# Kernel tuning notes

Measured on AMD Instinct MI355X. Metric: run time of the kernel, lower is better.

Reference implementation:

```python
import jax, jax.numpy as jnp
import numpy as np
import math

B, N, F, H = 16, 256, 1024, 16
HD = F // H  # head_dim = 64
NEG = -9e15


def setup_inputs() -> dict:
    key = jax.random.key(0)
    ks = jax.random.split(key, 12)
    s = 0.02
    return {
        "obj_feats": jax.random.normal(ks[0], (B, N, F), jnp.float32),
        "cross_feats": jax.random.normal(ks[1], (B, N, F), jnp.float32),
        "adj_matrix": jax.random.randint(ks[2], (B, N, N), 0, 2, jnp.int32),
        "label_biases_att": jax.random.normal(ks[3], (B, N, N), jnp.float32),
        "Wq": jax.random.normal(ks[4], (F, F), jnp.float32) * s,
        "bq": jnp.zeros((F,), jnp.float32),
        "Wk": jax.random.normal(ks[5], (F, F), jnp.float32) * s,
        "bk": jnp.zeros((F,), jnp.float32),
        "Wv": jax.random.normal(ks[6], (F, F), jnp.float32) * s,
        "bv": jnp.zeros((F,), jnp.float32),
        # grouped 1x1 conv: out=F, groups=H, in_per_group=F -> weight [F, F]
        "Wo": jax.random.normal(ks[7], (F, F), jnp.float32) * s,
        "bo": jnp.zeros((F,), jnp.float32),
    }


def reference(obj_feats, cross_feats, adj_matrix, label_biases_att,
              Wq, bq, Wk, bk, Wv, bv, Wo, bo):
    # projections (torch Linear: x @ W.T + b)
    q = (jnp.einsum('bnf,gf->bng', obj_feats, Wq) + bq).reshape(B, N, H, HD)
    k = (jnp.einsum('bnf,gf->bng', cross_feats, Wk) + bk).reshape(B, N, H, HD)
    v = jnp.einsum('bnf,gf->bng', cross_feats, Wv) + bv          # [B, N, F] (NOT split per head)

    scale = 1.0 / math.sqrt(float(HD))
    att = jnp.einsum('bqhd,bkhd->bqhk', q, k) * scale            # [B, Nq, H, Nk]

    # adjacency mask broadcast over heads + label bias (both indexed [b, q, k])
    mask = (adj_matrix > 0)[:, :, None, :]                       # [B, Nq, 1, Nk]
    att = jnp.where(mask, att, NEG) + label_biases_att[:, :, None, :]

    p = jax.nn.softmax(att, axis=-1)                             # softmax over keys

    # weighted sum against un-split values: [B, Nq, H, Nk] x [B, Nk, F]
    out = jnp.einsum('bqhk,bkf->bqhf', p, v)                     # [B, Nq, H, F]

    # grouped 1x1 conv: group h maps its F input channels -> HD output channels
    Wo_g = Wo.reshape(H, HD, F)
    out = jnp.einsum('bqhf,hdf->bqhd', out, Wo_g) + bo.reshape(H, HD)
    out = out.reshape(B, N, F)

    att_mean = p.sum(axis=2) / H                                 # [B, Nq, Nk]
    return out, att_mean
```

## Files before the change

### kernel.cpp

```cpp
#include <hip/hip_runtime.h>

#define NEGF -9e15f

typedef __attribute__((ext_vector_type(8))) unsigned short u16x8;
typedef __attribute__((ext_vector_type(8))) short          s16x8;
typedef __attribute__((ext_vector_type(4))) float          f32x4;

__device__ __forceinline__ unsigned short f2bf(float x) {
  union { float f; unsigned int u; } c; c.f = x;
  unsigned int r = c.u + 0x7fffu + ((c.u >> 16) & 1u);
  return (unsigned short)(r >> 16);
}
__device__ __forceinline__ float bf2f(unsigned short v) {
  union { float f; unsigned int u; } c; c.u = ((unsigned int)v) << 16;
  return c.f;
}

__device__ __forceinline__ void gload16(const void* g, void* l) {
  __builtin_amdgcn_global_load_lds(
      (const __attribute__((address_space(1))) unsigned int*)g,
      (__attribute__((address_space(3))) unsigned int*)l, 16, 0, 0);
}

__global__ __launch_bounds__(256) void cvt2_bf16(
    const float* __restrict__ a, const float* __restrict__ b,
    unsigned short* __restrict__ oa, unsigned short* __restrict__ ob)
{
  const int bid = blockIdx.x;
  const float* in = (bid < 4096) ? a : b;
  unsigned short* out = (bid < 4096) ? oa : ob;
  const int i = ((bid & 4095) * 256 + threadIdx.x) * 4;
  const float4 v = *(const float4*)(in + i);
  ushort4 o;
  o.x = f2bf(v.x); o.y = f2bf(v.y); o.z = f2bf(v.z); o.w = f2bf(v.w);
  *(ushort4*)(out + i) = o;
}

__global__ __launch_bounds__(256) void prep_w(
    const float* __restrict__ Wq, const float* __restrict__ Wk,
    const float* __restrict__ Wo, const float* __restrict__ Wv,
    unsigned short* __restrict__ Wall, unsigned short* __restrict__ Wo_bf,
    unsigned short* __restrict__ Wvt_bf)
{
  __shared__ float tile[32][33];
  const int bid = blockIdx.x;
  if (bid < 3072) {
    const int i = ((bid & 1023) * 256 + threadIdx.x) * 4;
    const float* in;
    unsigned short* out;
    float sc = 1.f;
    if (bid < 1024)      { in = Wq; out = Wall;           sc = 0.125f; }
    else if (bid < 2048) { in = Wk; out = Wall + 1048576; }
    else                 { in = Wo; out = Wo_bf; }
    const float4 v = *(const float4*)(in + i);
    ushort4 o;
    o.x = f2bf(v.x * sc); o.y = f2bf(v.y * sc);
    o.z = f2bf(v.z * sc); o.w = f2bf(v.w * sc);
    *(ushort4*)(out + i) = o;
  } else {
    const int j = bid - 3072;
    const int bc = (j & 31) * 32, br = (j >> 5) * 32;
    const int tx = threadIdx.x & 31, ty8 = threadIdx.x >> 5;
    #pragma unroll
    for (int jj = 0; jj < 32; jj += 8)
      tile[ty8 + jj][tx] = Wv[(size_t)(br + ty8 + jj) * 1024 + bc + tx];
    __syncthreads();
    #pragma unroll
    for (int jj = 0; jj < 32; jj += 8)
      Wvt_bf[(size_t)(bc + ty8 + jj) * 1024 + br + tx] = f2bf(tile[tx][ty8 + jj]);
  }
}

__global__ __launch_bounds__(256) void prep_bias(
    const float* __restrict__ bq, const float* __restrict__ bk,
    const float* __restrict__ Wo, const float* __restrict__ bv,
    float* __restrict__ ball)
{
  const int bid = blockIdx.x;
  if (bid < 4) {
    const int i = bid * 256 + threadIdx.x;
    ball[i]        = 0.125f * bq[i];
    ball[1024 + i] = bk[i];
  } else {
    const int g    = (bid - 4) * 4 + (threadIdx.x >> 6);
    const int lane = threadIdx.x & 63;
    float acc = 0.f;
    for (int f = lane; f < 1024; f += 64)
      acc = fmaf(Wo[(size_t)g * 1024 + f], bv[f], acc);
    #pragma unroll
    for (int off = 32; off > 0; off >>= 1) acc += __shfl_down(acc, off);
    if (lane == 0) ball[2048 + g] = acc;
  }
}

__global__ __launch_bounds__(256) void mb_prep(
    const int* __restrict__ adj, const float* __restrict__ lab,
    float* __restrict__ mb)
{
  const int i = (blockIdx.x * 256 + threadIdx.x) * 4;
  const int4   a = *(const int4*)(adj + i);
  const float4 l = *(const float4*)(lab + i);
  float4 o;
  o.x = a.x > 0 ? l.x : NEGF;
  o.y = a.y > 0 ? l.y : NEGF;
  o.z = a.z > 0 ? l.z : NEGF;
  o.w = a.w > 0 ? l.w : NEGF;
  *(float4*)(mb + i) = o;
}

__global__ __launch_bounds__(256, 3) void gemm_wov(
    const unsigned short* __restrict__ A,
    const unsigned short* __restrict__ Bw,
    unsigned short* __restrict__ Cout)
{
  __shared__ unsigned short Asm[128 * 64];
  __shared__ unsigned short Bsm[64 * 64];
  const int t = threadIdx.x;
  const int lane = t & 63, w = t >> 6;
  const int wm = w >> 1, wn = w & 1;
  const int bm = blockIdx.y * 128, bn = blockIdx.x * 64;

  const int srow = lane >> 3;
  const int skel = (lane & 7) * 8;
  const int fr = lane & 15, kf = (lane >> 4) * 8;

  f32x4 acc[4][2] = {};

  for (int k0 = 0; k0 < 1024; k0 += 64) {
    if (k0) __syncthreads();
    #pragma unroll
    for (int i = 0; i < 4; ++i) {
      const int c = i * 4 + w;
      const int r = c * 8 + srow;
      gload16(A + (size_t)(bm + r) * 1024 + k0 + skel, &Asm[c * 512]);
    }
    #pragma unroll
    for (int i = 0; i < 2; ++i) {
      const int c = i * 4 + w;
      const int r = c * 8 + srow;
      gload16(Bw + (size_t)(bn + r) * 1024 + k0 + skel, &Bsm[c * 512]);
    }
    __syncthreads();
    #pragma unroll
    for (int kk = 0; kk < 2; ++kk) {
      s16x8 af[4], bf[2];
      #pragma unroll
      for (int fm = 0; fm < 4; ++fm)
        af[fm] = *(const s16x8*)&Asm[(wm * 64 + fm * 16 + fr) * 64 + kk * 32 + kf];
      #pragma unroll
      for (int fn = 0; fn < 2; ++fn)
        bf[fn] = *(const s16x8*)&Bsm[(wn * 32 + fn * 16 + fr) * 64 + kk * 32 + kf];
      #pragma unroll
      for (int fm = 0; fm < 4; ++fm)
        #pragma unroll
        for (int fn = 0; fn < 2; ++fn)
          acc[fm][fn] = __builtin_amdgcn_mfma_f32_16x16x32_bf16(af[fm], bf[fn], acc[fm][fn], 0, 0, 0);
    }
  }

  const int rg = (lane >> 4) * 4;
  #pragma unroll
  for (int fm = 0; fm < 4; ++fm)
    #pragma unroll
    for (int fn = 0; fn < 2; ++fn) {
      const int col = bn + wn * 32 + fn * 16 + fr;
      #pragma unroll
      for (int r = 0; r < 4; ++r) {
        const int row = bm + wm * 64 + fm * 16 + rg + r;
        Cout[(size_t)row * 1024 + col] = f2bf(acc[fm][fn][r]);
      }
    }
}

__global__ __launch_bounds__(512, 2) void gemm_big(
    const unsigned short* __restrict__ objA,
    const unsigned short* __restrict__ crossA,
    const unsigned short* __restrict__ Wall,
    const float* __restrict__ ball,
    unsigned short* __restrict__ Qo,
    unsigned short* __restrict__ Ko,
    unsigned short* __restrict__ VWt)
{
  __shared__ __align__(16) char smem[131072];
  const int t = threadIdx.x;
  const int wid = t >> 6, lane = t & 63;
  const int wm = wid >> 2, wn = wid & 3;
  const int fr = lane & 15, grp = lane >> 4;

  const int bid = blockIdx.x;
  const int xcd = bid & 7, j = bid >> 3;
  const int bmi = (xcd >> 1) * 4 + j / 6;
  const int bni = (xcd & 1) * 6 + j % 6;
  const int bm = bmi * 256, bn = bni * 256;
  const unsigned short* Ag = ((bni < 4) ? objA : crossA) + (size_t)bm * 1024;
  const unsigned short* Bg = Wall + (size_t)bn * 1024;

  const int r8 = lane >> 3, cb = (lane & 7) * 16;

  f32x4 acc[8][4] = {};

  auto STAGE = [&](char* ldsbase, int k0) {
    #pragma unroll
    for (int i = 0; i < 4; ++i) {
      const int row = i * 64 + wid * 8 + r8;
      const int sc  = cb ^ ((row & 7) << 4);
      gload16((const char*)(Ag + (size_t)row * 1024 + k0) + sc,
              ldsbase + i * 8192 + wid * 1024);
      gload16((const char*)(Bg + (size_t)row * 1024 + k0) + sc,
              ldsbase + 32768 + i * 8192 + wid * 1024);
    }
  };

  auto COMPUTE = [&](const char* Ab) {
    const char* Bb = Ab + 32768;
    s16x8 bfr[4][2];
    #pragma unroll
    for (int fn = 0; fn < 4; ++fn)
      #pragma unroll
      for (int kk = 0; kk < 2; ++kk) {
        const int row = wn * 64 + fn * 16 + fr;
        bfr[fn][kk] = *(const s16x8*)(Bb + row * 128 + ((kk * 64 + grp * 16) ^ ((row & 7) << 4)));
      }
    #pragma unroll
    for (int qm = 0; qm < 2; ++qm) {
      s16x8 afr[4][2];
      #pragma unroll
      for (int fm2 = 0; fm2 < 4; ++fm2)
        #pragma unroll
        for (int kk = 0; kk < 2; ++kk) {
          const int row = wm * 128 + (qm * 4 + fm2) * 16 + fr;
          afr[fm2][kk] = *(const s16x8*)(Ab + row * 128 + ((kk * 64 + grp * 16) ^ ((row & 7) << 4)));
        }
      __builtin_amdgcn_s_setprio(1);
      #pragma unroll
      for (int fm2 = 0; fm2 < 4; ++fm2)
        #pragma unroll
        for (int fn = 0; fn < 4; ++fn) {
          acc[qm * 4 + fm2][fn] = __builtin_amdgcn_mfma_f32_16x16x32_bf16(
              afr[fm2][0], bfr[fn][0], acc[qm * 4 + fm2][fn], 0, 0, 0);
          acc[qm * 4 + fm2][fn] = __builtin_amdgcn_mfma_f32_16x16x32_bf16(
              afr[fm2][1], bfr[fn][1], acc[qm * 4 + fm2][fn], 0, 0, 0);
        }
      __builtin_amdgcn_s_setprio(0);
    }
  };

  STAGE(smem, 0);
  STAGE(smem + 65536, 64);

  #pragma unroll 2
  for (int kt = 0; kt < 14; ++kt) {
    asm volatile("s_waitcnt vmcnt(8)" ::: "memory");
    __builtin_amdgcn_s_barrier();
    asm volatile("" ::: "memory");
    COMPUTE(smem + (kt & 1) * 65536);
    asm volatile("" ::: "memory");
    __builtin_amdgcn_s_barrier();
    asm volatile("" ::: "memory");
    STAGE(smem + (kt & 1) * 65536, (kt + 2) * 64);
  }
  asm volatile("s_waitcnt vmcnt(8)" ::: "memory");
  __builtin_amdgcn_s_barrier();
  asm volatile("" ::: "memory");
  COMPUTE(smem);
  asm volatile("s_waitcnt vmcnt(0)" ::: "memory");
  __builtin_amdgcn_s_barrier();
  asm volatile("" ::: "memory");
  COMPUTE(smem + 65536);

  const int rg = grp * 4;
  const int mode = bn >> 10;
  #pragma unroll
  for (int fm = 0; fm < 8; ++fm) {
    #pragma unroll
    for (int fn = 0; fn < 4; ++fn) {
      const int col  = bn + wn * 64 + fn * 16 + fr;
      const int cl   = col & 1023;
      const float bb = ball[col];
      const int row0 = bm + wm * 128 + fm * 16 + rg;
      if (mode == 0) {
        #pragma unroll
        for (int r = 0; r < 4; ++r)
          Qo[(size_t)(row0 + r) * 1024 + cl] = f2bf(acc[fm][fn][r] + bb);
      } else if (mode == 1) {
        #pragma unroll
        for (int r = 0; r < 4; ++r)
          Ko[(size_t)(row0 + r) * 1024 + cl] = f2bf(acc[fm][fn][r] + bb);
      } else {
        const int bidx = row0 >> 8, tok = row0 & 255;
        ushort4 u;
        u.x = f2bf(acc[fm][fn][0] + bb);
        u.y = f2bf(acc[fm][fn][1] + bb);
        u.z = f2bf(acc[fm][fn][2] + bb);
        u.w = f2bf(acc[fm][fn][3] + bb);
        *(ushort4*)(VWt + ((size_t)bidx * 1024 + cl) * 256 + tok) = u;
      }
    }
  }
}

__global__ __launch_bounds__(256, 2) void attn_mfma(
    const unsigned short* __restrict__ Qg,
    const unsigned short* __restrict__ Kg,
    const unsigned short* __restrict__ VWt,
    const float* __restrict__ mb,
    const float* __restrict__ bo,
    float* __restrict__ outp, unsigned short* __restrict__ Pb)
{
  const int t = threadIdx.x;
  const int w = t >> 6, lane = t & 63;
  const int fr = lane & 15, grp = lane >> 4;
  const int bid = blockIdx.x;
  const int xcd = bid & 7, i = bid >> 3;
  const int h   = i & 15;
  const int bqt = xcd * 8 + (i >> 4);
  const int b   = bqt >> 2;
  const int qt  = bqt & 3;
  const int q0 = qt * 64 + w * 16;

  __shared__ __align__(16) unsigned short Ks[256 * 64];
  __shared__ __align__(16) unsigned short VWs[64 * 256];

  {
    const unsigned short* kb = Kg + (size_t)(b * 256) * 1024 + h * 64;
    const int colb = (lane & 7) * 16;
    #pragma unroll
    for (int c = 0; c < 8; ++c) {
      const int row = c * 32 + w * 8 + (lane >> 3);
      const int sb  = colb ^ ((row & 7) << 4);
      gload16(kb + (size_t)row * 1024 + (sb >> 1), (char*)Ks + c * 4096 + w * 1024);
    }
  }
  {
    const unsigned short* vwb = VWt + (size_t)(b * 16 + h) * 16384;
    const int xb = (lane & 31) * 16;
    #pragma unroll
    for (int c = 0; c < 8; ++c) {
      const int row = c * 8 + w * 2 + (lane >> 5);
      const int sb  = xb ^ ((row & 7) << 4);
      gload16(vwb + row * 256 + (sb >> 1), (char*)VWs + c * 4096 + w * 1024);
    }
  }

  const unsigned short* qp = Qg + ((size_t)(b * 256 + q0 + fr)) * 1024 + h * 64 + grp * 8;
  const s16x8 qf0 = *(const s16x8*)qp;
  const s16x8 qf1 = *(const s16x8*)(qp + 32);

  __syncthreads();

  const float* mbp = mb + ((size_t)(b * 256 + q0 + fr)) * 256 + grp * 4;
  const int colA = (grp * 16) ^ ((fr & 7) << 4);

  f32x4 s[16];
  #pragma unroll
  for (int nf = 0; nf < 16; ++nf) s[nf] = (f32x4){0.f, 0.f, 0.f, 0.f};

  s16x8 kA[8], kB[8];
  float4 mA[4], mB[4];
  float mx = -3e38f;

#define LOADB(KF, MF, nb)                                                    \
  { _Pragma("unroll") for (int i2 = 0; i2 < 4; ++i2) {                       \
      const char* rp = (const char*)Ks + (((nb)*4 + i2) * 16 + fr) * 128;    \
      KF[2*i2]   = *(const s16x8*)(rp + colA);                               \
      KF[2*i2+1] = *(const s16x8*)(rp + (colA ^ 64));                        \
      MF[i2]     = *(const float4*)(mbp + ((nb)*4 + i2) * 16); } }
#define MFMAB(KF, nb)                                                        \
  { _Pragma("unroll") for (int i2 = 0; i2 < 4; ++i2) {                       \
      s[(nb)*4+i2] = __builtin_amdgcn_mfma_f32_16x16x32_bf16(KF[2*i2],   qf0, s[(nb)*4+i2], 0, 0, 0); \
      s[(nb)*4+i2] = __builtin_amdgcn_mfma_f32_16x16x32_bf16(KF[2*i2+1], qf1, s[(nb)*4+i2], 0, 0, 0); } }
#define MASKB(MF, nb)                                                        \
  { _Pragma("unroll") for (int i2 = 0; i2 < 4; ++i2) {                       \
      _Pragma("unroll") for (int r = 0; r < 4; ++r) {                        \
        const float m = ((const float*)&MF[i2])[r];                          \
        const float v = (m > -1e14f) ? s[(nb)*4+i2][r] + m : m;              \
        s[(nb)*4+i2][r] = v; mx = fmaxf(mx, v); } } }

  LOADB(kA, mA, 0); LOADB(kB, mB, 1); MFMAB(kA, 0);
  MASKB(mA, 0);     LOADB(kA, mA, 2); MFMAB(kB, 1);
  MASKB(mB, 1);     LOADB(kB, mB, 3); MFMAB(kA, 2);
  MASKB(mA, 2);     LOADB(kA, mA, 4); MFMAB(kB, 3);
  MASKB(mB, 3);     LOADB(kB, mB, 5); MFMAB(kA, 4);
  MASKB(mA, 4);     LOADB(kA, mA, 6); MFMAB(kB, 5);
  MASKB(mB, 5);     LOADB(kB, mB, 7); MFMAB(kA, 6);
  MASKB(mA, 6);     MFMAB(kB, 7);     MASKB(mB, 7);
#undef LOADB
#undef MFMAB
#undef MASKB

  mx = fmaxf(mx, __shfl_xor(mx, 16));
  mx = fmaxf(mx, __shfl_xor(mx, 32));
  float sm = 0.f;
  #pragma unroll
  for (int nf = 0; nf < 16; ++nf)
    #pragma unroll
    for (int r = 0; r < 4; ++r) {
      const float e = __expf(s[nf][r] - mx);
      s[nf][r] = e;
      sm += e;
    }
  sm += __shfl_xor(sm, 16);
  sm += __shfl_xor(sm, 32);
  const float inv = 1.f / sm;

  uint2 u2[16];
  #pragma unroll
  for (int nf = 0; nf < 16; ++nf) {
    const unsigned lo = (unsigned)f2bf(s[nf][0] * inv) | ((unsigned)f2bf(s[nf][1] * inv) << 16);
    const unsigned hi = (unsigned)f2bf(s[nf][2] * inv) | ((unsigned)f2bf(s[nf][3] * inv) << 16);
    u2[nf] = make_uint2(lo, hi);
  }

  unsigned short* prow = Pb + (((size_t)(b * 16 + h)) * 256 + q0 + fr) * 256 + grp * 4;
  #pragma unroll
  for (int nf = 0; nf < 16; ++nf)
    *(uint2*)(prow + nf * 16) = u2[nf];

  f32x4 o[4];
  #pragma unroll
  for (int nf = 0; nf < 4; ++nf) o[nf] = (f32x4){0.f, 0.f, 0.f, 0.f};
  const int srcA = fr + ((grp & 1) << 5);
  const int srcB = srcA + 16;
  const int swz  = (fr & 7) << 4;
  const bool hiSel = (grp & 2);
  #pragma unroll
  for (int ks = 0; ks < 8; ++ks) {
    const int aLx = __shfl((int)u2[2 * ks].x,     srcA, 64);
    const int aLy = __shfl((int)u2[2 * ks].y,     srcA, 64);
    const int bLx = __shfl((int)u2[2 * ks].x,     srcB, 64);
    const int bLy = __shfl((int)u2[2 * ks].y,     srcB, 64);
    const int aHx = __shfl((int)u2[2 * ks + 1].x, srcA, 64);
    const int aHy = __shfl((int)u2[2 * ks + 1].y, srcA, 64);
    const int bHx = __shfl((int)u2[2 * ks + 1].x, srcB, 64);
    const int bHy = __shfl((int)u2[2 * ks + 1].y, srcB, 64);
    union { int4 i; s16x8 v; } pf;
    pf.i = hiSel ? make_int4(aHx, aHy, bHx, bHy) : make_int4(aLx, aLy, bLx, bLy);
    const int cbv = (ks * 64 + grp * 16) ^ swz;
    #pragma unroll
    for (int nf = 0; nf < 4; ++nf) {
      const s16x8 vf = *(const s16x8*)((const char*)VWs + (nf * 16 + fr) * 512 + cbv);
      o[nf] = __builtin_amdgcn_mfma_f32_16x16x32_bf16(pf.v, vf, o[nf], 0, 0, 0);
    }
  }

  #pragma unroll
  for (int nf = 0; nf < 4; ++nf) {
    const float bb = bo[h * 64 + nf * 16 + fr];
    #pragma unroll
    for (int r = 0; r < 4; ++r)
      outp[((size_t)b * 256 + q0 + grp * 4 + r) * 1024 + h * 64 + nf * 16 + fr]
          = o[nf][r] + bb;
  }
}

__global__ __launch_bounds__(256) void attm_reduce(
    const unsigned short* __restrict__ Pb, float* __restrict__ attm)
{
  const size_t idx = (size_t)blockIdx.x * 256 + threadIdx.x;
  const int    k8  = (int)(idx & 31);
  const size_t bq  = idx >> 5;
  const int    b   = (int)(bq >> 8);
  const int    q   = (int)(bq & 255);
  float s[8] = {};
  const unsigned short* base = Pb + (size_t)b * 1048576 + (size_t)q * 256 + k8 * 8;
  #pragma unroll
  for (int hh = 0; hh < 16; ++hh) {
    const u16x8 p = *(const u16x8*)(base + (size_t)hh * 65536);
    #pragma unroll
    for (int j = 0; j < 8; ++j) s[j] += bf2f(p[j]);
  }
  float* dst = attm + bq * 256 + k8 * 8;
  float4 r0, r1;
  r0.x = s[0] * 0.0625f; r0.y = s[1] * 0.0625f; r0.z = s[2] * 0.0625f; r0.w = s[3] * 0.0625f;
  r1.x = s[4] * 0.0625f; r1.y = s[5] * 0.0625f; r1.z = s[6] * 0.0625f; r1.w = s[7] * 0.0625f;
  *(float4*)dst = r0;
  *(float4*)(dst + 4) = r1;
}

extern "C" void kernel_launch(void* const* d_in, const int* in_sizes, int n_in,
                              void* d_out, int out_size, void* d_ws, size_t ws_size,
                              hipStream_t stream)
{
  const float* obj   = (const float*)d_in[0];
  const float* cross = (const float*)d_in[1];
  const int*   adj   = (const int*)d_in[2];
  const float* lab   = (const float*)d_in[3];
  const float* Wq    = (const float*)d_in[4];
  const float* bq    = (const float*)d_in[5];
  const float* Wk    = (const float*)d_in[6];
  const float* bk    = (const float*)d_in[7];
  const float* Wv    = (const float*)d_in[8];
  const float* bv    = (const float*)d_in[9];
  const float* Wo    = (const float*)d_in[10];
  const float* bo    = (const float*)d_in[11];

  float* out  = (float*)d_out;
  float* attm = out + (size_t)16 * 256 * 1024;

  char* ws = (char*)d_ws;
  unsigned short* obj_bf   = (unsigned short*)(ws + 0);
  unsigned short* cross_bf = (unsigned short*)(ws + 8388608);
  unsigned short* Qbf      = (unsigned short*)(ws + 16777216);
  unsigned short* Kbf      = (unsigned short*)(ws + 25165824);
  unsigned short* VWt      = (unsigned short*)(ws + 33554432);
  unsigned short* Wall     = (unsigned short*)(ws + 41943040);
  unsigned short* Wo_bf    = (unsigned short*)(ws + 48234496);
  unsigned short* Wvt_bf   = (unsigned short*)(ws + 50331648);
  float*          ball     = (float*)(ws + 50331648);
  unsigned short* Pbuf     = (unsigned short*)(ws + 52432896);
  float*          mbuf     = (float*)obj_bf;

  cvt2_bf16<<<8192, 256, 0, stream>>>(obj, cross, obj_bf, cross_bf);
  prep_w<<<4096, 256, 0, stream>>>(Wq, Wk, Wo, Wv, Wall, Wo_bf, Wvt_bf);

  gemm_wov<<<dim3(16, 8), 256, 0, stream>>>(Wo_bf, Wvt_bf, Wall + 2097152);

  prep_bias<<<260, 256, 0, stream>>>(bq, bk, Wo, bv, ball);

  gemm_big<<<192, 512, 0, stream>>>(
      obj_bf, cross_bf, Wall, ball, Qbf, Kbf, VWt);

  mb_prep<<<1024, 256, 0, stream>>>(adj, lab, mbuf);

  attn_mfma<<<1024, 256, 0, stream>>>(
      Qbf, Kbf, VWt, mbuf, bo, out, Pbuf);
  attm_reduce<<<512, 256, 0, stream>>>(Pbuf, attm);
}
```

Baseline: 120.5 us.

## Interleave per-chunk global-to-LDS loads with quarter-tile MFMA phases in projection GEMM

Replaces the monolithic stage-then-compute loop of the QKV projection GEMM with a finer-grained schedule. Each K tile is now split into four MFMA phases over A row quarters, and the next tile's A/B chunk loads are issued between those phases. The A chunks are split across iterations so the vmcnt wait still covers the data needed. The goal is to spread global-load issue across the compute and keep the MFMA pipes busy. The cost is many more workgroup barriers per tile, and the chunk ordering must line up exactly with the vmcnt accounting.

```diff
diff --git a/kernel.cpp b/kernel.cpp
--- a/kernel.cpp
+++ b/kernel.cpp
@@ -198,75 +198,84 @@
   const int r8 = lane >> 3, cb = (lane & 7) * 16;
 
   f32x4 acc[8][4] = {};
-
-  auto STAGE = [&](char* ldsbase, int k0) {
-    #pragma unroll
-    for (int i = 0; i < 4; ++i) {
-      const int row = i * 64 + wid * 8 + r8;
-      const int sc  = cb ^ ((row & 7) << 4);
-      gload16((const char*)(Ag + (size_t)row * 1024 + k0) + sc,
-              ldsbase + i * 8192 + wid * 1024);
-      gload16((const char*)(Bg + (size_t)row * 1024 + k0) + sc,
-              ldsbase + 32768 + i * 8192 + wid * 1024);
-    }
+  s16x8 bfr[4][2];
+  s16x8 aq[2][2];
+
+  auto CH = [&](int buf, int isB, int q, int k0) {
+    const int row = q * 64 + wid * 8 + r8;
+    const int sc  = cb ^ ((row & 7) << 4);
+    const unsigned short* src = isB ? Bg : Ag;
+    gload16((const char*)(src + (size_t)row * 1024 + k0) + sc,
+            smem + buf * 65536 + isB * 32768 + q * 8192 + wid * 1024);
   };
 
-  auto COMPUTE = [&](const char* Ab) {
-    const char* Bb = Ab + 32768;
-    s16x8 bfr[4][2];
-    #pragma unroll
-    for (int fn = 0; fn < 4; ++fn)
-      #pragma unroll
-      for (int kk = 0; kk < 2; ++kk) {
-        const int row = wn * 64 + fn * 16 + fr;
-        bfr[fn][kk] = *(const s16x8*)(Bb + row * 128 + ((kk * 64 + grp * 16) ^ ((row & 7) << 4)));
-      }
-    #pragma unroll
-    for (int qm = 0; qm < 2; ++qm) {
-      s16x8 afr[4][2];
-      #pragma unroll
-      for (int fm2 = 0; fm2 < 4; ++fm2)
-        #pragma unroll
-        for (int kk = 0; kk < 2; ++kk) {
-          const int row = wm * 128 + (qm * 4 + fm2) * 16 + fr;
-          afr[fm2][kk] = *(const s16x8*)(Ab + row * 128 + ((kk * 64 + grp * 16) ^ ((row & 7) << 4)));
-        }
-      __builtin_amdgcn_s_setprio(1);
-      #pragma unroll
-      for (int fm2 = 0; fm2 < 4; ++fm2)
-        #pragma unroll
-        for (int fn = 0; fn < 4; ++fn) {
-          acc[qm * 4 + fm2][fn] = __builtin_amdgcn_mfma_f32_16x16x32_bf16(
-              afr[fm2][0], bfr[fn][0], acc[qm * 4 + fm2][fn], 0, 0, 0);
-          acc[qm * 4 + fm2][fn] = __builtin_amdgcn_mfma_f32_16x16x32_bf16(
-              afr[fm2][1], bfr[fn][1], acc[qm * 4 + fm2][fn], 0, 0, 0);
-        }
-      __builtin_amdgcn_s_setprio(0);
-    }
-  };
-
-  STAGE(smem, 0);
-  STAGE(smem + 65536, 64);
+#define BAR() { asm volatile("" ::: "memory"); __builtin_amdgcn_s_barrier(); asm volatile("" ::: "memory"); }
+#define RDB(BUF)                                                             \
+  { _Pragma("unroll") for (int fn = 0; fn < 4; ++fn)                         \
+      _Pragma("unroll") for (int kk = 0; kk < 2; ++kk) {                     \
+        const int row = wn * 64 + fn * 16 + fr;                              \
+        bfr[fn][kk] = *(const s16x8*)((BUF) + 32768 + row * 128 +            \
+            ((kk * 64 + grp * 16) ^ ((row & 7) << 4)));                      \
+      } }
+#define RDA(BUF, P)                                                          \
+  { _Pragma("unroll") for (int fm = 0; fm < 2; ++fm)                         \
+      _Pragma("unroll") for (int kk = 0; kk < 2; ++kk) {                     \
+        const int row = wm * 128 + (2 * (P) + fm) * 16 + fr;                 \
+        aq[fm][kk] = *(const s16x8*)((BUF) + row * 128 +                     \
+            ((kk * 64 + grp * 16) ^ ((row & 7) << 4)));                      \
+      } }
+#define MMQ(P)                                                               \
+  { __builtin_amdgcn_s_setprio(1);                                           \
+    _Pragma("unroll") for (int fm = 0; fm < 2; ++fm)                         \
+      _Pragma("unroll") for (int fn = 0; fn < 4; ++fn) {                     \
+        acc[2 * (P) + fm][fn] = __builtin_amdgcn_mfma_f32_16x16x32_bf16(     \
+            aq[fm][0], bfr[fn][0], acc[2 * (P) + fm][fn], 0, 0, 0);          \
+        acc[2 * (P) + fm][fn] = __builtin_amdgcn_mfma_f32_16x16x32_bf16(     \
+            aq[fm][1], bfr[fn][1], acc[2 * (P) + fm][fn], 0, 0, 0);          \
+      }                                                                      \
+    __builtin_amdgcn_s_setprio(0); }
+#define TILE4(BUF)                                                           \
+  RDB(BUF); RDA(BUF, 0); BAR(); MMQ(0); BAR();                               \
+  RDA(BUF, 1); BAR(); MMQ(1); BAR();                                         \
+  RDA(BUF, 2); BAR(); MMQ(2); BAR();                                         \
+  RDA(BUF, 3); BAR(); MMQ(3); BAR();
+
+  CH(0, 1, 0, 0); CH(0, 1, 1, 0); CH(0, 1, 2, 0); CH(0, 1, 3, 0);
+  CH(0, 0, 0, 0); CH(0, 0, 1, 0); CH(0, 0, 2, 0); CH(0, 0, 3, 0);
+  CH(1, 1, 0, 64); CH(1, 1, 1, 64); CH(1, 1, 2, 64); CH(1, 1, 3, 64);
+  CH(1, 0, 0, 64); CH(1, 0, 2, 64);
 
   #pragma unroll 2
   for (int kt = 0; kt < 14; ++kt) {
+    const int cur = kt & 1;
+    char* bufc = smem + cur * 65536;
+    const int k1 = (kt + 1) * 64, k2 = (kt + 2) * 64;
+    CH(cur ^ 1, 0, 1, k1);
+    CH(cur ^ 1, 0, 3, k1);
     asm volatile("s_waitcnt vmcnt(8)" ::: "memory");
-    __builtin_amdgcn_s_barrier();
-    asm volatile("" ::: "memory");
-    COMPUTE(smem + (kt & 1) * 65536);
-    asm volatile("" ::: "memory");
-    __builtin_amdgcn_s_barrier();
-    asm volatile("" ::: "memory");
-    STAGE(smem + (kt & 1) * 65536, (kt + 2) * 64);
-  }
+    BAR();
+    RDB(bufc); RDA(bufc, 0);
+    BAR(); MMQ(0); BAR();
+    RDA(bufc, 1); CH(cur, 1, 0, k2); CH(cur, 1, 1, k2);
+    BAR(); MMQ(1); BAR();
+    RDA(bufc, 2); CH(cur, 1, 2, k2); CH(cur, 1, 3, k2);
+    BAR(); MMQ(2); BAR();
+    RDA(bufc, 3); CH(cur, 0, 0, k2); CH(cur, 0, 2, k2);
+    BAR(); MMQ(3); BAR();
+  }
+  CH(1, 0, 1, 960); CH(1, 0, 3, 960);
   asm volatile("s_waitcnt vmcnt(8)" ::: "memory");
-  __builtin_amdgcn_s_barrier();
-  asm volatile("" ::: "memory");
-  COMPUTE(smem);
+  BAR();
+  TILE4(smem);
   asm volatile("s_waitcnt vmcnt(0)" ::: "memory");
-  __builtin_amdgcn_s_barrier();
-  asm volatile("" ::: "memory");
-  COMPUTE(smem + 65536);
+  BAR();
+  TILE4(smem + 65536);
+
+#undef BAR
+#undef RDB
+#undef RDA
+#undef MMQ
+#undef TILE4
 
   const int rg = grp * 4;
   const int mode = bn >> 10;
```

Result: faster. 118.1 us (-2.0%).
